# Kernel optimization log

Measured on AMD Instinct MI355X. Metric: run time of the kernel, lower is better.

## Reference

```python
import jax, jax.numpy as jnp
import numpy as np

EPS_RMS = 1.1920929e-07  # torch F.rms_norm default eps = finfo(float32).eps
N_EMBD = 64
N_QKV = 256


def _silu(t):
    return t * jax.nn.sigmoid(t)


def _rms_norm(t):
    return t * jax.lax.rsqrt(jnp.mean(t * t, axis=-1, keepdims=True) + EPS_RMS)


def _w_norm(w, n):
    target_std = n ** (-0.5)
    return w * (target_std / (jnp.std(w, ddof=1) + 1e-08))


def setup_inputs() -> dict:
    key = jax.random.key(0)
    ks = jax.random.split(key, 7)
    B, T = 8, 8192
    x = jax.random.normal(ks[0], (B, T, N_EMBD), dtype=jnp.float32)
    y = jax.random.normal(ks[1], (B, T, N_QKV), dtype=jnp.float32)
    # CastedLinear init: uniform(-s, s), s = sqrt(3)/sqrt(in_features)
    def lin(k, out_f, in_f):
        s = (3.0 ** 0.5) * in_f ** (-0.5)
        return jax.random.uniform(k, (out_f, in_f), jnp.float32, -s, s)
    w_qkv = lin(ks[2], 3 * N_QKV, N_EMBD)          # [768, 64]
    w_swiglu = lin(ks[3], 2 * N_EMBD, N_QKV)       # [128, 256]
    w_out = lin(ks[4], N_EMBD, N_EMBD)             # [64, 64]
    out_w = lin(ks[5], N_EMBD, N_EMBD)             # self.out weight [64, 64]
    tao = lin(ks[6], 3, 1)                          # [3, 1]
    return {"x": x, "y": y, "w_qkv": w_qkv, "w_swiglu": w_swiglu,
            "w_out": w_out, "out_w": out_w, "tao": tao}


def reference(x, y, w_qkv, w_swiglu, w_out, out_w, tao):
    B = x.shape[0]
    # SwiGLU branch: F.linear(y, w_swiglu) -> [B,T,2*n_embd], chunk
    uv = jnp.einsum('btq,eq->bte', y, w_swiglu)
    u, v = jnp.split(uv, 2, axis=-1)                 # each [B,T,64]
    y_out = x + jnp.einsum('btd,ed->bte', u * _silu(v), w_out)

    # gates
    g = jnp.clip(jnp.abs(tao), 1e-08, 1.0)           # [3,1]
    alpha, beta, gamma = g[0], g[1], g[2]

    # Hebbian outer-product memory: mean_b(u^T v) * n_embd^-0.5, rms-normed
    ao = jnp.einsum('btd,bte->de', u, v) / B * (N_EMBD ** (-0.5))  # [64,64]
    ao = _rms_norm(ao)

    # update w_qkv
    n1 = _silu(w_qkv @ ao)                            # [768,64]
    w_qkv_new = _w_norm(w_qkv + n1 @ out_w.T, N_EMBD) * alpha

    # update w_swiglu: view(64, 512).T @ ao
    n2 = _silu(w_swiglu.reshape(N_EMBD, 2 * N_QKV).T @ ao)  # [512,64]
    n2 = n2 @ out_w.T                                  # [512,64]
    w_swiglu_new = w_swiglu + n2.T.reshape(2 * N_EMBD, N_QKV)
    w_swiglu_new = _w_norm(w_swiglu_new, N_QKV) * beta

    # update w_out
    n3 = _silu(w_out @ ao)                             # [64,64]
    w_out_new = _w_norm(w_out + n3 @ out_w.T, N_QKV) * gamma

    return (y_out, w_qkv_new, w_swiglu_new, w_out_new)
```

## Files before the change

kernel.cpp:

```cpp
#include <hip/hip_runtime.h>
#include <cstdint>

typedef short short8 __attribute__((ext_vector_type(8)));
typedef short short4_t __attribute__((ext_vector_type(4)));
typedef float floatx4 __attribute__((ext_vector_type(4)));

#define MFMA_BF16 __builtin_amdgcn_mfma_f32_16x16x32_bf16

__device__ __forceinline__ short f2bf(float f) {
  union { float f; unsigned u; } a; a.f = f;
  unsigned r = a.u + 0x7FFFu + ((a.u >> 16) & 1u);
  return (short)(r >> 16);
}
__device__ __forceinline__ float bf2f(short s) {
  union { unsigned u; float f; } a;
  a.u = ((unsigned)(unsigned short)s) << 16;
  return a.f;
}
__device__ __forceinline__ float silu_f(float v) {
  return v / (1.0f + __expf(-v));
}

#define QDIM 256
#define DEMB 64
#define TILE_T 32
#define ITERS 4
#define NBLK1 512
#define YSTR 264
#define TSTR 40
#define HSTR 72

#define OFF_QKV 4194304
#define OFF_SW  4243456
#define OFF_WO  4276224

#define AO_COPIES 16
#define WS_SUMS   65536
#define WS_AOT    65544
#define WS_W1P    67592
#define WS_W2P    83976

__global__ __launch_bounds__(256) void k0_pack(
    const float* __restrict__ w_sw, const float* __restrict__ w_out,
    short* __restrict__ W1P, short* __restrict__ W2P)
{
  int t = blockIdx.x * 256 + threadIdx.x;
  if (t < 4096) {
    int lane = t & 63, kt = (t >> 6) & 7, ntw = t >> 9;
    int row = (ntw >> 1) * 32 + (ntw & 1) * 16 + (lane & 15);
    int col = kt * 32 + (lane >> 4) * 8;
    const float* p = w_sw + row * QDIM + col;
    short8 f;
#pragma unroll
    for (int j = 0; j < 8; ++j) f[j] = f2bf(p[j]);
    ((short8*)W1P)[t] = f;
  } else {
    int u = t - 4096;
    int lane = u & 63, ktw = u >> 6;
    int row = (ktw >> 1) * 16 + (lane & 15);
    int col = (ktw & 1) * 32 + (lane >> 4) * 8;
    const float* p = w_out + row * DEMB + col;
    short8 f;
#pragma unroll
    for (int j = 0; j < 8; ++j) f[j] = f2bf(p[j]);
    ((short8*)W2P)[u] = f;
  }
}

__global__ __launch_bounds__(256, 2) void k1_main(
    const float* __restrict__ x, const float* __restrict__ y,
    const short* __restrict__ W1P, const short* __restrict__ W2P,
    float* __restrict__ y_out, float* __restrict__ ao_copies)
{
  __shared__ __align__(16) short Ylds[2][TILE_T * YSTR];
  __shared__ __align__(16) short UVT[128 * TSTR];
  __shared__ __align__(16) short Hlds[TILE_T * HSTR];

  const int tid  = threadIdx.x;
  const int lane = tid & 63;
  const int wave = tid >> 6;
  const int l15  = lane & 15;
  const int quad = lane >> 4;
  const floatx4 fzero = {0.f, 0.f, 0.f, 0.f};
  const int tok0 = blockIdx.x * (TILE_T * ITERS);

  const short8* W1v = (const short8*)W1P;
  const short8* W2v = (const short8*)W2P;
  short8 b1[2][8];
#pragma unroll
  for (int nt = 0; nt < 2; ++nt)
#pragma unroll
    for (int kt = 0; kt < 8; ++kt)
      b1[nt][kt] = W1v[((wave * 2 + nt) * 8 + kt) * 64 + lane];
  short8 b2[2];
#pragma unroll
  for (int kt = 0; kt < 2; ++kt)
    b2[kt] = W2v[(wave * 2 + kt) * 64 + lane];

  floatx4 ao_acc[4];
#pragma unroll
  for (int i = 0; i < 4; ++i) ao_acc[i] = fzero;

  float4 yreg[8];
  {
    const float4* src = (const float4*)(y + (size_t)tok0 * QDIM);
#pragma unroll
    for (int rep = 0; rep < 8; ++rep) yreg[rep] = src[tid + rep * 256];
#pragma unroll
    for (int rep = 0; rep < 8; ++rep) {
      int i = tid + rep * 256;
      int tok = i >> 6;
      int col = (i & 63) * 4;
      float4 f = yreg[rep];
      short4_t p4 = { f2bf(f.x), f2bf(f.y), f2bf(f.z), f2bf(f.w) };
      *(short4_t*)&Ylds[0][tok * YSTR + col] = p4;
    }
  }
  float xreg[8];
  __syncthreads();

  for (int it = 0; it < ITERS; ++it) {
    const int cur = it & 1;

    if (it + 1 < ITERS) {
      const float4* src = (const float4*)(y + (size_t)(tok0 + (it + 1) * TILE_T) * QDIM);
#pragma unroll
      for (int rep = 0; rep < 8; ++rep) yreg[rep] = src[tid + rep * 256];
    }
    if (it > 0) {
      const int tb = tok0 + (it - 1) * TILE_T;
#pragma unroll
      for (int mt = 0; mt < 2; ++mt) {
        floatx4 acc2 = fzero;
#pragma unroll
        for (int kt = 0; kt < 2; ++kt) {
          short8 a2 = *(const short8*)&Hlds[(mt * 16 + l15) * HSTR + kt * 32 + quad * 8];
          acc2 = MFMA_BF16(a2, b2[kt], acc2, 0, 0, 0);
        }
        int e = wave * 16 + l15;
#pragma unroll
        for (int r = 0; r < 4; ++r) {
          size_t idx = (size_t)(tb + mt * 16 + quad * 4 + r) * DEMB + e;
          y_out[idx] = xreg[mt * 4 + r] + acc2[r];
        }
      }
    }
    floatx4 acc[2][2];
#pragma unroll
    for (int a = 0; a < 2; ++a)
#pragma unroll
      for (int b = 0; b < 2; ++b) acc[a][b] = fzero;
#pragma unroll
    for (int kt = 0; kt < 8; ++kt) {
      short8 a0 = *(const short8*)&Ylds[cur][(l15)      * YSTR + kt * 32 + quad * 8];
      short8 a1 = *(const short8*)&Ylds[cur][(16 + l15) * YSTR + kt * 32 + quad * 8];
      acc[0][0] = MFMA_BF16(a0, b1[0][kt], acc[0][0], 0, 0, 0);
      acc[0][1] = MFMA_BF16(a0, b1[1][kt], acc[0][1], 0, 0, 0);
      acc[1][0] = MFMA_BF16(a1, b1[0][kt], acc[1][0], 0, 0, 0);
      acc[1][1] = MFMA_BF16(a1, b1[1][kt], acc[1][1], 0, 0, 0);
    }
#pragma unroll
    for (int mt = 0; mt < 2; ++mt)
#pragma unroll
      for (int nt = 0; nt < 2; ++nt) {
        short4_t p4;
#pragma unroll
        for (int r = 0; r < 4; ++r) p4[r] = f2bf(acc[mt][nt][r]);
        int c  = wave * 32 + nt * 16 + l15;
        int t0 = mt * 16 + quad * 4;
        *(short4_t*)&UVT[c * TSTR + t0] = p4;
      }
    __syncthreads();

    {
      const float* xb = x + (size_t)(tok0 + it * TILE_T) * DEMB + wave * 16 + l15;
#pragma unroll
      for (int mt = 0; mt < 2; ++mt)
#pragma unroll
        for (int r = 0; r < 4; ++r)
          xreg[mt * 4 + r] = xb[(mt * 16 + quad * 4 + r) * DEMB];
    }
    {
      int d  = tid & 63;
      int t0 = (tid >> 6) * 8;
      short8 u8 = *(const short8*)&UVT[d * TSTR + t0];
      short8 v8 = *(const short8*)&UVT[(64 + d) * TSTR + t0];
#pragma unroll
      for (int j = 0; j < 8; ++j) {
        float h = bf2f(u8[j]) * silu_f(bf2f(v8[j]));
        Hlds[(t0 + j) * HSTR + d] = f2bf(h);
      }
    }
    {
      short8 a3 = *(const short8*)&UVT[(wave * 16 + l15) * TSTR + quad * 8];
#pragma unroll
      for (int et = 0; et < 4; ++et) {
        short8 b3 = *(const short8*)&UVT[(64 + et * 16 + l15) * TSTR + quad * 8];
        ao_acc[et] = MFMA_BF16(a3, b3, ao_acc[et], 0, 0, 0);
      }
    }
    if (it + 1 < ITERS) {
#pragma unroll
      for (int rep = 0; rep < 8; ++rep) {
        int i = tid + rep * 256;
        int tok = i >> 6;
        int col = (i & 63) * 4;
        float4 f = yreg[rep];
        short4_t p4 = { f2bf(f.x), f2bf(f.y), f2bf(f.z), f2bf(f.w) };
        *(short4_t*)&Ylds[1 - cur][tok * YSTR + col] = p4;
      }
    }
    __syncthreads();
  }

  {
    const int tb = tok0 + (ITERS - 1) * TILE_T;
#pragma unroll
    for (int mt = 0; mt < 2; ++mt) {
      floatx4 acc2 = fzero;
#pragma unroll
      for (int kt = 0; kt < 2; ++kt) {
        short8 a2 = *(const short8*)&Hlds[(mt * 16 + l15) * HSTR + kt * 32 + quad * 8];
        acc2 = MFMA_BF16(a2, b2[kt], acc2, 0, 0, 0);
      }
      int e = wave * 16 + l15;
#pragma unroll
      for (int r = 0; r < 4; ++r) {
        size_t idx = (size_t)(tb + mt * 16 + quad * 4 + r) * DEMB + e;
        y_out[idx] = xreg[mt * 4 + r] + acc2[r];
      }
    }
  }

  float* dst = ao_copies + (blockIdx.x & (AO_COPIES - 1)) * 4096;
#pragma unroll
  for (int et = 0; et < 4; ++et)
#pragma unroll
    for (int r = 0; r < 4; ++r) {
      int d = wave * 16 + quad * 4 + r;
      int e = et * 16 + l15;
      atomicAdd(&dst[d * 64 + e], ao_acc[et][r]);
    }
}

__global__ __launch_bounds__(256) void k2_finalize(
    const float* __restrict__ ao_copies, unsigned short* __restrict__ aoT)
{
  __shared__ float aoFT[64 * 65];
  __shared__ float ssPart[256];
  __shared__ float scRow[64];
  const int tid = threadIdx.x;

#pragma unroll
  for (int k = 0; k < 16; ++k) {
    int idx = k * 256 + tid;
    float v = 0.f;
#pragma unroll
    for (int c = 0; c < AO_COPIES; ++c) v += ao_copies[c * 4096 + idx];
    v *= (1.0f / 64.0f);
    int d = idx >> 6, e = idx & 63;
    aoFT[e * 65 + d] = v;
  }
  __syncthreads();
  {
    int d = tid >> 2, q = tid & 3;
    float ssp = 0.f;
#pragma unroll
    for (int e2 = 0; e2 < 16; ++e2) {
      float v = aoFT[(q * 16 + e2) * 65 + d];
      ssp += v * v;
    }
    ssPart[tid] = ssp;
  }
  __syncthreads();
  if (tid < 64) {
    float ss = ssPart[tid * 4] + ssPart[tid * 4 + 1] +
               ssPart[tid * 4 + 2] + ssPart[tid * 4 + 3];
    scRow[tid] = rsqrtf(ss * (1.0f / 64.0f) + 1.1920929e-07f);
  }
  __syncthreads();
#pragma unroll
  for (int k = 0; k < 16; ++k) {
    int j = k * 256 + tid;
    int e = j >> 6, d = j & 63;
    aoT[j] = (unsigned short)f2bf(aoFT[e * 65 + d] * scRow[d]);
  }
}

__global__ __launch_bounds__(64) void k3_updates(
    const float* __restrict__ w_qkv, const float* __restrict__ w_sw,
    const float* __restrict__ w_out, const float* __restrict__ out_w,
    const unsigned short* __restrict__ aoT, float* __restrict__ out,
    float* __restrict__ sums)
{
  __shared__ __align__(16) short Nlds[16 * 72];
  const int lane = threadIdx.x;
  const int l15  = lane & 15;
  const int quad = lane >> 4;
  const int rid  = blockIdx.x;
  const floatx4 fzero = {0.f, 0.f, 0.f, 0.f};
  const short8* aoTv = (const short8*)aoT;

  short8 bf[2][4];
#pragma unroll
  for (int kt = 0; kt < 2; ++kt)
#pragma unroll
    for (int nt = 0; nt < 4; ++nt)
      bf[kt][nt] = aoTv[(nt * 16 + l15) * 8 + kt * 4 + quad];

  short8 af[2];
  if (rid < 48) {
    const float* wr = w_qkv + (size_t)(rid * 16 + l15) * 64;
#pragma unroll
    for (int kt = 0; kt < 2; ++kt) {
      const float* p = wr + kt * 32 + quad * 8;
      short8 f;
#pragma unroll
      for (int j = 0; j < 8; ++j) f[j] = f2bf(p[j]);
      af[kt] = f;
    }
  } else if (rid < 80) {
    int p0 = (rid - 48) * 16;
#pragma unroll
    for (int kt = 0; kt < 2; ++kt) {
      short8 f;
#pragma unroll
      for (int j = 0; j < 8; ++j) {
        int a = kt * 32 + quad * 8 + j;
        f[j] = f2bf(w_sw[a * 512 + p0 + l15]);
      }
      af[kt] = f;
    }
  } else {
    const float* wr = w_out + (size_t)((rid - 80) * 16 + l15) * 64;
#pragma unroll
    for (int kt = 0; kt < 2; ++kt) {
      const float* p = wr + kt * 32 + quad * 8;
      short8 f;
#pragma unroll
      for (int j = 0; j < 8; ++j) f[j] = f2bf(p[j]);
      af[kt] = f;
    }
  }

  floatx4 acc[4];
#pragma unroll
  for (int nt = 0; nt < 4; ++nt) acc[nt] = fzero;
#pragma unroll
  for (int kt = 0; kt < 2; ++kt)
#pragma unroll
    for (int nt = 0; nt < 4; ++nt)
      acc[nt] = MFMA_BF16(af[kt], bf[kt][nt], acc[nt], 0, 0, 0);
#pragma unroll
  for (int nt = 0; nt < 4; ++nt)
#pragma unroll
    for (int r = 0; r < 4; ++r)
      Nlds[(quad * 4 + r) * 72 + nt * 16 + l15] = f2bf(silu_f(acc[nt][r]));
  __syncthreads();

  float s1 = 0.f, s2 = 0.f;
  int matrix;

  if (rid < 48 || rid >= 80) {
    matrix = (rid < 48) ? 0 : 2;
    short8 a2[2];
#pragma unroll
    for (int kt = 0; kt < 2; ++kt)
      a2[kt] = *(const short8*)&Nlds[l15 * 72 + kt * 32 + quad * 8];
    short8 b2[2][4];
#pragma unroll
    for (int nt = 0; nt < 4; ++nt) {
      const float* wr = out_w + (size_t)(nt * 16 + l15) * 64;
#pragma unroll
      for (int kt = 0; kt < 2; ++kt) {
        const float* p = wr + kt * 32 + quad * 8;
        short8 f;
#pragma unroll
        for (int j = 0; j < 8; ++j) f[j] = f2bf(p[j]);
        b2[kt][nt] = f;
      }
    }
    floatx4 acc2[4];
#pragma unroll
    for (int nt = 0; nt < 4; ++nt) acc2[nt] = fzero;
#pragma unroll
    for (int kt = 0; kt < 2; ++kt)
#pragma unroll
      for (int nt = 0; nt < 4; ++nt)
        acc2[nt] = MFMA_BF16(a2[kt], b2[kt][nt], acc2[nt], 0, 0, 0);

    const float* Wsrc = (rid < 48) ? w_qkv : w_out;
    int base_row = (rid < 48) ? rid * 16 : (rid - 80) * 16;
    int off      = (rid < 48) ? OFF_QKV : OFF_WO;
#pragma unroll
    for (int nt = 0; nt < 4; ++nt)
#pragma unroll
      for (int r = 0; r < 4; ++r) {
        int row = base_row + quad * 4 + r;
        int col = nt * 16 + l15;
        float val = Wsrc[row * 64 + col] + acc2[nt][r];
        out[off + row * 64 + col] = val;
        s1 += val; s2 += val * val;
      }
  } else {
    matrix = 1;
    int p0 = (rid - 48) * 16;
    short8 b2[2];
#pragma unroll
    for (int kt = 0; kt < 2; ++kt)
      b2[kt] = *(const short8*)&Nlds[l15 * 72 + kt * 32 + quad * 8];
    short8 a2[4][2];
#pragma unroll
    for (int mt = 0; mt < 4; ++mt) {
      const float* wr = out_w + (size_t)(mt * 16 + l15) * 64;
#pragma unroll
      for (int kt = 0; kt < 2; ++kt) {
        const float* p = wr + kt * 32 + quad * 8;
        short8 f;
#pragma unroll
        for (int j = 0; j < 8; ++j) f[j] = f2bf(p[j]);
        a2[mt][kt] = f;
      }
    }
    floatx4 acc2[4];
#pragma unroll
    for (int mt = 0; mt < 4; ++mt) acc2[mt] = fzero;
#pragma unroll
    for (int mt = 0; mt < 4; ++mt)
#pragma unroll
      for (int kt = 0; kt < 2; ++kt)
        acc2[mt] = MFMA_BF16(a2[mt][kt], b2[kt], acc2[mt], 0, 0, 0);
#pragma unroll
    for (int mt = 0; mt < 4; ++mt)
#pragma unroll
      for (int r = 0; r < 4; ++r) {
        int a = mt * 16 + quad * 4 + r;
        int p = p0 + l15;
        int idx = a * 512 + p;
        float val = w_sw[idx] + acc2[mt][r];
        out[OFF_SW + idx] = val;
        s1 += val; s2 += val * val;
      }
  }

#pragma unroll
  for (int off = 32; off > 0; off >>= 1) {
    s1 += __shfl_down(s1, off);
    s2 += __shfl_down(s2, off);
  }
  if (lane == 0) {
    atomicAdd(&sums[matrix * 2],     s1);
    atomicAdd(&sums[matrix * 2 + 1], s2);
  }
}

__global__ __launch_bounds__(256) void k4_scale(
    float* __restrict__ out, const float* __restrict__ sums,
    const float* __restrict__ tao)
{
  int i = blockIdx.x * 256 + threadIdx.x;
  int matrix, idx; float N, tstd;
  if (i < 49152)      { matrix = 0; idx = OFF_QKV + i;           N = 49152.f; tstd = 0.125f;  }
  else if (i < 81920) { matrix = 1; idx = OFF_SW + (i - 49152);  N = 32768.f; tstd = 0.0625f; }
  else                { matrix = 2; idx = OFF_WO + (i - 81920);  N = 4096.f;  tstd = 0.0625f; }
  float sum = sums[matrix * 2], sumsq = sums[matrix * 2 + 1];
  float mean = sum / N;
  float var  = (sumsq - N * mean * mean) / (N - 1.f);
  float sd   = sqrtf(fmaxf(var, 0.f));
  float g    = fminf(fmaxf(fabsf(tao[matrix]), 1e-8f), 1.0f);
  out[idx] *= g * tstd / (sd + 1e-8f);
}

extern "C" void kernel_launch(void* const* d_in, const int* in_sizes, int n_in,
                              void* d_out, int out_size, void* d_ws, size_t ws_size,
                              hipStream_t stream) {
  const float* x     = (const float*)d_in[0];
  const float* y     = (const float*)d_in[1];
  const float* w_qkv = (const float*)d_in[2];
  const float* w_sw  = (const float*)d_in[3];
  const float* w_out = (const float*)d_in[4];
  const float* out_w = (const float*)d_in[5];
  const float* tao   = (const float*)d_in[6];
  float* out = (float*)d_out;
  float* ws  = (float*)d_ws;

  float* ao_copies    = ws;
  float* sums         = ws + WS_SUMS;
  unsigned short* aoT = (unsigned short*)(ws + WS_AOT);
  short* W1P          = (short*)(ws + WS_W1P);
  short* W2P          = (short*)(ws + WS_W2P);

  hipMemsetAsync(d_ws, 0, (WS_SUMS + 8) * sizeof(float), stream);
  k0_pack<<<dim3(18), dim3(256), 0, stream>>>(w_sw, w_out, W1P, W2P);
  k1_main<<<dim3(NBLK1), dim3(256), 0, stream>>>(x, y, W1P, W2P, out, ao_copies);
  k2_finalize<<<dim3(1), dim3(256), 0, stream>>>(ao_copies, aoT);
  k3_updates<<<dim3(84), dim3(64), 0, stream>>>(w_qkv, w_sw, w_out, out_w,
                                                aoT, out, sums);
  k4_scale<<<dim3(336), dim3(256), 0, stream>>>(out, sums, tao);
}
```

Measured before the change: 143.0 us.

## Fuse weight packing into main kernel and merge tail kernels via grid barrier

```diff
diff --git a/kernel.cpp b/kernel.cpp
--- a/kernel.cpp
+++ b/kernel.cpp
@@ -36,40 +36,10 @@
 
 #define AO_COPIES 16
 #define WS_SUMS   65536
-#define WS_AOT    65544
-#define WS_W1P    67592
-#define WS_W2P    83976
-
-__global__ __launch_bounds__(256) void k0_pack(
-    const float* __restrict__ w_sw, const float* __restrict__ w_out,
-    short* __restrict__ W1P, short* __restrict__ W2P)
-{
-  int t = blockIdx.x * 256 + threadIdx.x;
-  if (t < 4096) {
-    int lane = t & 63, kt = (t >> 6) & 7, ntw = t >> 9;
-    int row = (ntw >> 1) * 32 + (ntw & 1) * 16 + (lane & 15);
-    int col = kt * 32 + (lane >> 4) * 8;
-    const float* p = w_sw + row * QDIM + col;
-    short8 f;
-#pragma unroll
-    for (int j = 0; j < 8; ++j) f[j] = f2bf(p[j]);
-    ((short8*)W1P)[t] = f;
-  } else {
-    int u = t - 4096;
-    int lane = u & 63, ktw = u >> 6;
-    int row = (ktw >> 1) * 16 + (lane & 15);
-    int col = (ktw & 1) * 32 + (lane >> 4) * 8;
-    const float* p = w_out + row * DEMB + col;
-    short8 f;
-#pragma unroll
-    for (int j = 0; j < 8; ++j) f[j] = f2bf(p[j]);
-    ((short8*)W2P)[u] = f;
-  }
-}
 
 __global__ __launch_bounds__(256, 2) void k1_main(
     const float* __restrict__ x, const float* __restrict__ y,
-    const short* __restrict__ W1P, const short* __restrict__ W2P,
+    const float* __restrict__ w_sw, const float* __restrict__ w_out,
     float* __restrict__ y_out, float* __restrict__ ao_copies)
 {
   __shared__ __align__(16) short Ylds[2][TILE_T * YSTR];
@@ -84,28 +54,42 @@
   const floatx4 fzero = {0.f, 0.f, 0.f, 0.f};
   const int tok0 = blockIdx.x * (TILE_T * ITERS);
 
-  const short8* W1v = (const short8*)W1P;
-  const short8* W2v = (const short8*)W2P;
-  short8 b1[2][8];
-#pragma unroll
-  for (int nt = 0; nt < 2; ++nt)
-#pragma unroll
-    for (int kt = 0; kt < 8; ++kt)
-      b1[nt][kt] = W1v[((wave * 2 + nt) * 8 + kt) * 64 + lane];
-  short8 b2[2];
-#pragma unroll
-  for (int kt = 0; kt < 2; ++kt)
-    b2[kt] = W2v[(wave * 2 + kt) * 64 + lane];
-
-  floatx4 ao_acc[4];
-#pragma unroll
-  for (int i = 0; i < 4; ++i) ao_acc[i] = fzero;
-
   float4 yreg[8];
   {
     const float4* src = (const float4*)(y + (size_t)tok0 * QDIM);
 #pragma unroll
     for (int rep = 0; rep < 8; ++rep) yreg[rep] = src[tid + rep * 256];
+  }
+
+  short8 b1[2][8];
+#pragma unroll
+  for (int nt = 0; nt < 2; ++nt) {
+    const float* wr = w_sw + (size_t)(wave * 32 + nt * 16 + l15) * QDIM + quad * 8;
+#pragma unroll
+    for (int kt = 0; kt < 8; ++kt) {
+      float4 f0 = *(const float4*)(wr + kt * 32);
+      float4 f1 = *(const float4*)(wr + kt * 32 + 4);
+      short8 f = { f2bf(f0.x), f2bf(f0.y), f2bf(f0.z), f2bf(f0.w),
+                   f2bf(f1.x), f2bf(f1.y), f2bf(f1.z), f2bf(f1.w) };
+      b1[nt][kt] = f;
+    }
+  }
+  short8 b2[2];
+#pragma unroll
+  for (int kt = 0; kt < 2; ++kt) {
+    const float* wr = w_out + (size_t)(wave * 16 + l15) * DEMB + kt * 32 + quad * 8;
+    float4 f0 = *(const float4*)(wr);
+    float4 f1 = *(const float4*)(wr + 4);
+    short8 f = { f2bf(f0.x), f2bf(f0.y), f2bf(f0.z), f2bf(f0.w),
+                 f2bf(f1.x), f2bf(f1.y), f2bf(f1.z), f2bf(f1.w) };
+    b2[kt] = f;
+  }
+
+  floatx4 ao_acc[4];
+#pragma unroll
+  for (int i = 0; i < 4; ++i) ao_acc[i] = fzero;
+
+  {
 #pragma unroll
     for (int rep = 0; rep < 8; ++rep) {
       int i = tid + rep * 256;
@@ -243,12 +227,17 @@
     }
 }
 
-__global__ __launch_bounds__(256) void k2_finalize(
-    const float* __restrict__ ao_copies, unsigned short* __restrict__ aoT)
+__global__ __launch_bounds__(256) void k3_fused(
+    const float* __restrict__ w_qkv, const float* __restrict__ w_sw,
+    const float* __restrict__ w_out, const float* __restrict__ out_w,
+    const float* __restrict__ ao_copies, const float* __restrict__ tao,
+    float* __restrict__ out, float* __restrict__ sums,
+    unsigned* __restrict__ cnt)
 {
   __shared__ float aoFT[64 * 65];
   __shared__ float ssPart[256];
   __shared__ float scRow[64];
+  __shared__ __align__(16) short Nlds[4][16 * 72];
   const int tid = threadIdx.x;
 
 #pragma unroll
@@ -279,34 +268,27 @@
     scRow[tid] = rsqrtf(ss * (1.0f / 64.0f) + 1.1920929e-07f);
   }
   __syncthreads();
-#pragma unroll
-  for (int k = 0; k < 16; ++k) {
-    int j = k * 256 + tid;
-    int e = j >> 6, d = j & 63;
-    aoT[j] = (unsigned short)f2bf(aoFT[e * 65 + d] * scRow[d]);
-  }
-}
-
-__global__ __launch_bounds__(64) void k3_updates(
-    const float* __restrict__ w_qkv, const float* __restrict__ w_sw,
-    const float* __restrict__ w_out, const float* __restrict__ out_w,
-    const unsigned short* __restrict__ aoT, float* __restrict__ out,
-    float* __restrict__ sums)
-{
-  __shared__ __align__(16) short Nlds[16 * 72];
-  const int lane = threadIdx.x;
+
+  const int lane = tid & 63;
+  const int wave = tid >> 6;
   const int l15  = lane & 15;
   const int quad = lane >> 4;
-  const int rid  = blockIdx.x;
+  const int rid  = blockIdx.x * 4 + wave;
   const floatx4 fzero = {0.f, 0.f, 0.f, 0.f};
-  const short8* aoTv = (const short8*)aoT;
 
   short8 bf[2][4];
 #pragma unroll
   for (int kt = 0; kt < 2; ++kt)
 #pragma unroll
-    for (int nt = 0; nt < 4; ++nt)
-      bf[kt][nt] = aoTv[(nt * 16 + l15) * 8 + kt * 4 + quad];
+    for (int nt = 0; nt < 4; ++nt) {
+      short8 f;
+#pragma unroll
+      for (int j = 0; j < 8; ++j) {
+        int d = kt * 32 + quad * 8 + j;
+        f[j] = f2bf(aoFT[(nt * 16 + l15) * 65 + d] * scRow[d]);
+      }
+      bf[kt][nt] = f;
+    }
 
   short8 af[2];
   if (rid < 48) {
@@ -355,19 +337,20 @@
   for (int nt = 0; nt < 4; ++nt)
 #pragma unroll
     for (int r = 0; r < 4; ++r)
-      Nlds[(quad * 4 + r) * 72 + nt * 16 + l15] = f2bf(silu_f(acc[nt][r]));
+      Nlds[wave][(quad * 4 + r) * 72 + nt * 16 + l15] = f2bf(silu_f(acc[nt][r]));
   __syncthreads();
 
   float s1 = 0.f, s2 = 0.f;
   int matrix;
+  float vals[16];
 
   if (rid < 48 || rid >= 80) {
     matrix = (rid < 48) ? 0 : 2;
     short8 a2[2];
 #pragma unroll
     for (int kt = 0; kt < 2; ++kt)
-      a2[kt] = *(const short8*)&Nlds[l15 * 72 + kt * 32 + quad * 8];
-    short8 b2[2][4];
+      a2[kt] = *(const short8*)&Nlds[wave][l15 * 72 + kt * 32 + quad * 8];
+    short8 b2w[2][4];
 #pragma unroll
     for (int nt = 0; nt < 4; ++nt) {
       const float* wr = out_w + (size_t)(nt * 16 + l15) * 64;
@@ -377,7 +360,7 @@
         short8 f;
 #pragma unroll
         for (int j = 0; j < 8; ++j) f[j] = f2bf(p[j]);
-        b2[kt][nt] = f;
+        b2w[kt][nt] = f;
       }
     }
     floatx4 acc2[4];
@@ -387,11 +370,10 @@
     for (int kt = 0; kt < 2; ++kt)
 #pragma unroll
       for (int nt = 0; nt < 4; ++nt)
-        acc2[nt] = MFMA_BF16(a2[kt], b2[kt][nt], acc2[nt], 0, 0, 0);
+        acc2[nt] = MFMA_BF16(a2[kt], b2w[kt][nt], acc2[nt], 0, 0, 0);
 
     const float* Wsrc = (rid < 48) ? w_qkv : w_out;
     int base_row = (rid < 48) ? rid * 16 : (rid - 80) * 16;
-    int off      = (rid < 48) ? OFF_QKV : OFF_WO;
 #pragma unroll
     for (int nt = 0; nt < 4; ++nt)
 #pragma unroll
@@ -399,17 +381,17 @@
         int row = base_row + quad * 4 + r;
         int col = nt * 16 + l15;
         float val = Wsrc[row * 64 + col] + acc2[nt][r];
-        out[off + row * 64 + col] = val;
+        vals[nt * 4 + r] = val;
         s1 += val; s2 += val * val;
       }
   } else {
     matrix = 1;
     int p0 = (rid - 48) * 16;
-    short8 b2[2];
+    short8 b2s[2];
 #pragma unroll
     for (int kt = 0; kt < 2; ++kt)
-      b2[kt] = *(const short8*)&Nlds[l15 * 72 + kt * 32 + quad * 8];
-    short8 a2[4][2];
+      b2s[kt] = *(const short8*)&Nlds[wave][l15 * 72 + kt * 32 + quad * 8];
+    short8 a2w[4][2];
 #pragma unroll
     for (int mt = 0; mt < 4; ++mt) {
       const float* wr = out_w + (size_t)(mt * 16 + l15) * 64;
@@ -419,7 +401,7 @@
         short8 f;
 #pragma unroll
         for (int j = 0; j < 8; ++j) f[j] = f2bf(p[j]);
-        a2[mt][kt] = f;
+        a2w[mt][kt] = f;
       }
     }
     floatx4 acc2[4];
@@ -429,16 +411,14 @@
     for (int mt = 0; mt < 4; ++mt)
 #pragma unroll
       for (int kt = 0; kt < 2; ++kt)
-        acc2[mt] = MFMA_BF16(a2[mt][kt], b2[kt], acc2[mt], 0, 0, 0);
+        acc2[mt] = MFMA_BF16(a2w[mt][kt], b2s[kt], acc2[mt], 0, 0, 0);
 #pragma unroll
     for (int mt = 0; mt < 4; ++mt)
 #pragma unroll
       for (int r = 0; r < 4; ++r) {
         int a = mt * 16 + quad * 4 + r;
-        int p = p0 + l15;
-        int idx = a * 512 + p;
-        float val = w_sw[idx] + acc2[mt][r];
-        out[OFF_SW + idx] = val;
+        float val = w_sw[a * 512 + p0 + l15] + acc2[mt][r];
+        vals[mt * 4 + r] = val;
         s1 += val; s2 += val * val;
       }
   }
@@ -451,24 +431,45 @@
   if (lane == 0) {
     atomicAdd(&sums[matrix * 2],     s1);
     atomicAdd(&sums[matrix * 2 + 1], s2);
-  }
-}
-
-__global__ __launch_bounds__(256) void k4_scale(
-    float* __restrict__ out, const float* __restrict__ sums,
-    const float* __restrict__ tao)
-{
-  int i = blockIdx.x * 256 + threadIdx.x;
-  int matrix, idx; float N, tstd;
-  if (i < 49152)      { matrix = 0; idx = OFF_QKV + i;           N = 49152.f; tstd = 0.125f;  }
-  else if (i < 81920) { matrix = 1; idx = OFF_SW + (i - 49152);  N = 32768.f; tstd = 0.0625f; }
-  else                { matrix = 2; idx = OFF_WO + (i - 81920);  N = 4096.f;  tstd = 0.0625f; }
-  float sum = sums[matrix * 2], sumsq = sums[matrix * 2 + 1];
-  float mean = sum / N;
-  float var  = (sumsq - N * mean * mean) / (N - 1.f);
+    __hip_atomic_fetch_add(cnt, 1u, __ATOMIC_RELEASE, __HIP_MEMORY_SCOPE_AGENT);
+  }
+  while (__hip_atomic_load(cnt, __ATOMIC_ACQUIRE, __HIP_MEMORY_SCOPE_AGENT) < 84u) {
+    __builtin_amdgcn_s_sleep(1);
+  }
+
+  float ssum = __hip_atomic_load(&sums[matrix * 2],
+                                 __ATOMIC_RELAXED, __HIP_MEMORY_SCOPE_AGENT);
+  float ssq  = __hip_atomic_load(&sums[matrix * 2 + 1],
+                                 __ATOMIC_RELAXED, __HIP_MEMORY_SCOPE_AGENT);
+  float N    = (matrix == 0) ? 49152.f : (matrix == 1) ? 32768.f : 4096.f;
+  float tstd = (matrix == 0) ? 0.125f : 0.0625f;
+  float mean = ssum / N;
+  float var  = (ssq - N * mean * mean) / (N - 1.f);
   float sd   = sqrtf(fmaxf(var, 0.f));
   float g    = fminf(fmaxf(fabsf(tao[matrix]), 1e-8f), 1.0f);
-  out[idx] *= g * tstd / (sd + 1e-8f);
+  float scale = g * tstd / (sd + 1e-8f);
+
+  if (rid < 48 || rid >= 80) {
+    int base_row = (rid < 48) ? rid * 16 : (rid - 80) * 16;
+    int off2     = (rid < 48) ? OFF_QKV : OFF_WO;
+#pragma unroll
+    for (int nt = 0; nt < 4; ++nt)
+#pragma unroll
+      for (int r = 0; r < 4; ++r) {
+        int row = base_row + quad * 4 + r;
+        int col = nt * 16 + l15;
+        out[off2 + row * 64 + col] = vals[nt * 4 + r] * scale;
+      }
+  } else {
+    int p0 = (rid - 48) * 16;
+#pragma unroll
+    for (int mt = 0; mt < 4; ++mt)
+#pragma unroll
+      for (int r = 0; r < 4; ++r) {
+        int a = mt * 16 + quad * 4 + r;
+        out[OFF_SW + a * 512 + p0 + l15] = vals[mt * 4 + r] * scale;
+      }
+  }
 }
 
 extern "C" void kernel_launch(void* const* d_in, const int* in_sizes, int n_in,
@@ -484,17 +485,12 @@
   float* out = (float*)d_out;
   float* ws  = (float*)d_ws;
 
-  float* ao_copies    = ws;
-  float* sums         = ws + WS_SUMS;
-  unsigned short* aoT = (unsigned short*)(ws + WS_AOT);
-  short* W1P          = (short*)(ws + WS_W1P);
-  short* W2P          = (short*)(ws + WS_W2P);
+  float* ao_copies = ws;
+  float* sums      = ws + WS_SUMS;
+  unsigned* cnt    = (unsigned*)(ws + WS_SUMS + 7);
 
   hipMemsetAsync(d_ws, 0, (WS_SUMS + 8) * sizeof(float), stream);
-  k0_pack<<<dim3(18), dim3(256), 0, stream>>>(w_sw, w_out, W1P, W2P);
-  k1_main<<<dim3(NBLK1), dim3(256), 0, stream>>>(x, y, W1P, W2P, out, ao_copies);
-  k2_finalize<<<dim3(1), dim3(256), 0, stream>>>(ao_copies, aoT);
-  k3_updates<<<dim3(84), dim3(64), 0, stream>>>(w_qkv, w_sw, w_out, out_w,
-                                                aoT, out, sums);
-  k4_scale<<<dim3(336), dim3(256), 0, stream>>>(out, sums, tao);
-}
+  k1_main<<<dim3(NBLK1), dim3(256), 0, stream>>>(x, y, w_sw, w_out, out, ao_copies);
+  k3_fused<<<dim3(21), dim3(256), 0, stream>>>(w_qkv, w_sw, w_out, out_w,
+                                               ao_copies, tao, out, sums, cnt);
+}
```

Measured after the change: 146.4 us. +2.4%, slower.
